# Kernel optimization log

Measured on AMD Instinct MI355X. Metric: run time of the kernel, lower is better.

Reference implementation:

```python
import jax, jax.numpy as jnp
import numpy as np

EMBED_DIM = 512
BATCH = 4
SEQ = 4096

def setup_inputs() -> dict:
    key = jax.random.key(0)
    k1, k2, k3, k4 = jax.random.split(key, 4)
    inputs = jax.random.normal(k1, (BATCH, SEQ, EMBED_DIM), dtype=jnp.float32)
    scale = 1.0 / np.sqrt(EMBED_DIM)
    Wq = jax.random.normal(k2, (EMBED_DIM, EMBED_DIM), dtype=jnp.float32) * scale
    Wk = jax.random.normal(k3, (EMBED_DIM, EMBED_DIM), dtype=jnp.float32) * scale
    Wv = jax.random.normal(k4, (EMBED_DIM, EMBED_DIM), dtype=jnp.float32) * scale
    temperature = jnp.float32(1.0)
    return {"inputs": inputs, "Wq": Wq, "Wk": Wk, "Wv": Wv, "temperature": temperature}

def reference(inputs, Wq, Wk, Wv, temperature):
    # nn.Linear with weight W computes x @ W.T; we store W as (out,in)-equivalent square,
    # applied as x @ W.T for faithfulness.
    Q = jnp.einsum('bsd,ed->bse', inputs, Wq)
    K = jnp.einsum('bsd,ed->bse', inputs, Wk)
    V = jnp.einsum('bsd,ed->bse', inputs, Wv)
    d = inputs.shape[-1]
    scores = jnp.einsum('bqe,bke->bqk', Q, K) * (temperature / jnp.sqrt(jnp.float32(d)))  # [B,S,S]
    attn = jax.nn.softmax(scores, axis=-1)
    return jnp.einsum('bqk,bke->bqe', attn, V)
```

## Files before the change

### kernel.cpp

```cpp
#include <hip/hip_runtime.h>
#include <hip/hip_bf16.h>
#include <stdint.h>

typedef __bf16 bf16;
typedef bf16 bf16x8 __attribute__((ext_vector_type(8)));
typedef bf16 bf16x4 __attribute__((ext_vector_type(4)));
typedef float f32x4 __attribute__((ext_vector_type(4)));

#define MFMA16(a, b, c) __builtin_amdgcn_mfma_f32_16x16x32_bf16((a), (b), (c), 0, 0, 0)

__device__ __forceinline__ void async_ld16(bf16* lds, const bf16* g) {
    __builtin_amdgcn_global_load_lds(
        (const __attribute__((address_space(1))) void*)g,
        (__attribute__((address_space(3))) void*)lds, 16, 0, 0);
}

__global__ __launch_bounds__(256) void proj_kernel(
    const float* __restrict__ X,
    const float* __restrict__ Wq,
    const float* __restrict__ Wk,
    const float* __restrict__ Wv,
    bf16* __restrict__ Qo,
    bf16* __restrict__ Ko,
    bf16* __restrict__ Vt)
{
    __shared__ bf16 As[128][72];
    __shared__ bf16 Bs[128][72];

    const int z    = blockIdx.z;
    const float* W = (z == 0) ? Wq : (z == 1) ? Wk : Wv;
    const int row0 = blockIdx.x * 128;
    const int col0 = blockIdx.y * 128;

    const int t    = threadIdx.x;
    const int w    = t >> 6;
    const int lane = t & 63;
    const int lg   = lane >> 4;
    const int lc   = lane & 15;
    const int wr   = (w >> 1) * 64;
    const int wc   = (w & 1) * 64;

    const int srow = t >> 1;
    const int sd0  = (t & 1) * 16;

    f32x4 acc[4][4];
    for (int a = 0; a < 4; ++a)
        for (int b = 0; b < 4; ++b)
            acc[a][b] = (f32x4){0.f, 0.f, 0.f, 0.f};

    for (int kt = 0; kt < 16; ++kt) {
        const int k = kt * 32;
        __syncthreads();
        {
            const float* xs = X + (size_t)(row0 + srow) * 512 + k + sd0;
            float4 a0 = *(const float4*)(xs + 0);
            float4 a1 = *(const float4*)(xs + 4);
            float4 a2 = *(const float4*)(xs + 8);
            float4 a3 = *(const float4*)(xs + 12);
            bf16x8 h0 = { (bf16)a0.x, (bf16)a0.y, (bf16)a0.z, (bf16)a0.w,
                          (bf16)a1.x, (bf16)a1.y, (bf16)a1.z, (bf16)a1.w };
            bf16x8 h1 = { (bf16)a2.x, (bf16)a2.y, (bf16)a2.z, (bf16)a2.w,
                          (bf16)a3.x, (bf16)a3.y, (bf16)a3.z, (bf16)a3.w };
            *(bf16x8*)&As[srow][sd0]     = h0;
            *(bf16x8*)&As[srow][sd0 + 8] = h1;

            const float* ws_ = W + (size_t)(col0 + srow) * 512 + k + sd0;
            float4 b0 = *(const float4*)(ws_ + 0);
            float4 b1 = *(const float4*)(ws_ + 4);
            float4 b2 = *(const float4*)(ws_ + 8);
            float4 b3 = *(const float4*)(ws_ + 12);
            bf16x8 g0 = { (bf16)b0.x, (bf16)b0.y, (bf16)b0.z, (bf16)b0.w,
                          (bf16)b1.x, (bf16)b1.y, (bf16)b1.z, (bf16)b1.w };
            bf16x8 g1 = { (bf16)b2.x, (bf16)b2.y, (bf16)b2.z, (bf16)b2.w,
                          (bf16)b3.x, (bf16)b3.y, (bf16)b3.z, (bf16)b3.w };
            *(bf16x8*)&Bs[srow][sd0]     = g0;
            *(bf16x8*)&Bs[srow][sd0 + 8] = g1;
        }
        __syncthreads();

        bf16x8 af[4], bfr[4];
        for (int fr = 0; fr < 4; ++fr)
            af[fr] = *(const bf16x8*)&As[wr + fr * 16 + lc][lg * 8];
        for (int fc = 0; fc < 4; ++fc)
            bfr[fc] = *(const bf16x8*)&Bs[wc + fc * 16 + lc][lg * 8];
        for (int fr = 0; fr < 4; ++fr)
            for (int fc = 0; fc < 4; ++fc)
                acc[fr][fc] = MFMA16(af[fr], bfr[fc], acc[fr][fc]);
    }

    if (z < 2) {
        bf16* outp = (z == 0) ? Qo : Ko;
        for (int fr = 0; fr < 4; ++fr)
            for (int fc = 0; fc < 4; ++fc) {
                const int colg = col0 + wc + fc * 16 + lc;
                const int rowb = row0 + wr + fr * 16 + lg * 4;
                for (int i = 0; i < 4; ++i)
                    outp[(size_t)(rowb + i) * 512 + colg] = (bf16)acc[fr][fc][i];
            }
    } else {
        for (int fr = 0; fr < 4; ++fr)
            for (int fc = 0; fc < 4; ++fc) {
                const int e    = col0 + wc + fc * 16 + lc;
                const int rowb = row0 + wr + fr * 16 + lg * 4;
                const int bb   = rowb >> 12;
                const int sl   = rowb & 4095;
                bf16x4 v = { (bf16)acc[fr][fc][0], (bf16)acc[fr][fc][1],
                             (bf16)acc[fr][fc][2], (bf16)acc[fr][fc][3] };
                *(bf16x4*)&Vt[(((size_t)(bb * 512 + e)) << 12) + sl] = v;
            }
    }
}

__global__ __launch_bounds__(512) void flash_kernel(
    const bf16* __restrict__ Q,
    const bf16* __restrict__ K,
    const bf16* __restrict__ Vt,
    const float* __restrict__ temp,
    float* __restrict__ Out)
{
    extern __shared__ char smem[];
    bf16* Kb = (bf16*)smem;
    bf16* Pb = (bf16*)(smem + 2 * 64 * 512 * 2);
    __shared__ float l_part[64][2];

    const int b  = blockIdx.y;
    const int q0 = blockIdx.x * 64;
    const int t    = threadIdx.x;
    const int w    = t >> 6;
    const int lane = t & 63;
    const int lg   = lane >> 4;
    const int lc   = lane & 15;
    const int qrb  = (w >> 1) * 16;
    const int par  = w & 1;

    const float scale2 = temp[0] * 0.04419417382415922f * 1.4426950408889634f;

    const bf16* kbase = K  + (size_t)b * 4096 * 512;
    const bf16* vbase = Vt + (size_t)b * 512 * 4096;

    bf16x8 qf[16];
    {
        const bf16* qrow = Q + ((size_t)(b * 4096 + q0 + qrb + lc)) * 512 + lg * 8;
#pragma unroll
        for (int kt = 0; kt < 16; ++kt)
            qf[kt] = *(const bf16x8*)(qrow + kt * 32);
    }

    f32x4 acc[4][4];
    for (int a = 0; a < 4; ++a)
        for (int c = 0; c < 4; ++c)
            acc[a][c] = (f32x4){0.f, 0.f, 0.f, 0.f};
    float Lacc[4] = {0.f, 0.f, 0.f, 0.f};

#pragma unroll
    for (int j = 0; j < 8; ++j) {
        const int r = w * 8 + j;
        async_ld16(Kb + (size_t)r * 512,
                   kbase + (size_t)r * 512 + ((lane ^ j) << 3));
    }
    __syncthreads();

    const int r7  = lc & 7;
    const int xlo = (lg ^ (r7 & 3)) << 3;
    const int xb2 = (r7 & 4) << 3;

    for (int kv0 = 0; kv0 < 4096; kv0 += 64) {
        const int cur = (kv0 >> 6) & 1;
        const bf16* Kc = Kb + (size_t)cur * 32768;
        bf16*       Pc = Pb + (size_t)cur * (64 * 72);

        if (kv0 + 64 < 4096) {
            bf16* Kn = Kb + (size_t)(cur ^ 1) * 32768;
            const bf16* knx = kbase + (size_t)(kv0 + 64) * 512;
#pragma unroll
            for (int j = 0; j < 8; ++j) {
                const int r = w * 8 + j;
                async_ld16(Kn + (size_t)r * 512,
                           knx + (size_t)r * 512 + ((lane ^ j) << 3));
            }
        }

        const bf16* vb0 = vbase + (size_t)(w * 64 + lc) * 4096 + kv0 + lg * 8;
        bf16x8 vv[8];
#pragma unroll
        for (int kk2 = 0; kk2 < 2; ++kk2)
#pragma unroll
            for (int fc = 0; fc < 4; ++fc)
                vv[kk2 * 4 + fc] =
                    *(const bf16x8*)(vb0 + (size_t)fc * 16 * 4096 + kk2 * 32);

        f32x4 s0 = (f32x4){0.f, 0.f, 0.f, 0.f};
        f32x4 s1 = (f32x4){0.f, 0.f, 0.f, 0.f};
        const bf16* kr0 = Kc + (size_t)(par * 32 + lc) * 512 + xlo;
        const bf16* kr1 = kr0 + (size_t)16 * 512;
#pragma unroll
        for (int kt = 0; kt < 16; ++kt) {
            const int off = (kt * 32) ^ xb2;
            bf16x8 k0 = *(const bf16x8*)(kr0 + off);
            bf16x8 k1 = *(const bf16x8*)(kr1 + off);
            s0 = MFMA16(qf[kt], k0, s0);
            s1 = MFMA16(qf[kt], k1, s1);
        }

#pragma unroll
        for (int i = 0; i < 4; ++i) {
            const int row = qrb + lg * 4 + i;
            float p0 = __builtin_amdgcn_exp2f(s0[i] * scale2);
            float p1 = __builtin_amdgcn_exp2f(s1[i] * scale2);
            Pc[row * 72 + par * 32 + lc]      = (bf16)p0;
            Pc[row * 72 + par * 32 + 16 + lc] = (bf16)p1;
            Lacc[i] += p0 + p1;
        }

        __syncthreads();

#pragma unroll
        for (int kk2 = 0; kk2 < 2; ++kk2) {
            bf16x8 pa[4];
#pragma unroll
            for (int fr = 0; fr < 4; ++fr)
                pa[fr] = *(const bf16x8*)&Pc[(fr * 16 + lc) * 72 + kk2 * 32 + lg * 8];
#pragma unroll
            for (int fc = 0; fc < 4; ++fc)
#pragma unroll
                for (int fr = 0; fr < 4; ++fr)
                    acc[fr][fc] = MFMA16(pa[fr], vv[kk2 * 4 + fc], acc[fr][fc]);
        }
    }

#pragma unroll
    for (int d = 1; d < 16; d <<= 1)
#pragma unroll
        for (int i = 0; i < 4; ++i)
            Lacc[i] += __shfl_xor(Lacc[i], d);
    if (lc == 0)
#pragma unroll
        for (int i = 0; i < 4; ++i)
            l_part[qrb + lg * 4 + i][par] = Lacc[i];
    __syncthreads();

    for (int fr = 0; fr < 4; ++fr) {
        float invl[4];
#pragma unroll
        for (int i = 0; i < 4; ++i) {
            const int row = fr * 16 + lg * 4 + i;
            invl[i] = 1.0f / (l_part[row][0] + l_part[row][1]);
        }
        for (int fc = 0; fc < 4; ++fc) {
            const size_t base =
                ((size_t)(b * 4096 + q0 + fr * 16 + lg * 4)) * 512 + w * 64 + fc * 16 + lc;
#pragma unroll
            for (int i = 0; i < 4; ++i)
                Out[base + (size_t)i * 512] = acc[fr][fc][i] * invl[i];
        }
    }
}

extern "C" void kernel_launch(void* const* d_in, const int* in_sizes, int n_in,
                              void* d_out, int out_size, void* d_ws, size_t ws_size,
                              hipStream_t stream) {
    const float* X    = (const float*)d_in[0];
    const float* Wq   = (const float*)d_in[1];
    const float* Wk   = (const float*)d_in[2];
    const float* Wv   = (const float*)d_in[3];
    const float* temp = (const float*)d_in[4];
    float* Out = (float*)d_out;

    const size_t NE = (size_t)4 * 4096 * 512;
    bf16* Qw = (bf16*)d_ws;
    bf16* Kw = Qw + NE;
    bf16* Vt = Kw + NE;

    proj_kernel<<<dim3(128, 4, 3), 256, 0, stream>>>(X, Wq, Wk, Wv, Qw, Kw, Vt);

    const size_t smem_bytes = (size_t)2 * 64 * 512 * 2 + (size_t)2 * 64 * 72 * 2;
    flash_kernel<<<dim3(64, 4), 512, smem_bytes, stream>>>(Qw, Kw, Vt, temp, Out);
}
```

Baseline: 281.3 us.

## Remap flash blocks across XCDs and replace syncthreads with targeted waitcnt barriers

Flattens the flash grid to 1D and remaps block index to (batch, q-tile) so that blocks sharing a batch's K/V land on the same XCDs, for better L2 reuse. It replaces the full __syncthreads with explicit vmcnt/lgkmcnt waits plus s_barrier, so the V register loads and the next K prefetch stay in flight across the barrier. It also issues the first K tile load before the Q fragment loads and shrinks the P buffer to a single copy. The prefetch is now unconditional, so the last iteration wastes one K tile load, and correctness depends on the hand-counted vmcnt value.

Measured after the change: 308.2 us. 9.6% more time.

```diff
diff --git a/kernel.cpp b/kernel.cpp
--- a/kernel.cpp
+++ b/kernel.cpp
@@ -123,8 +123,10 @@
     bf16* Pb = (bf16*)(smem + 2 * 64 * 512 * 2);
     __shared__ float l_part[64][2];
 
-    const int b  = blockIdx.y;
-    const int q0 = blockIdx.x * 64;
+    const int L  = blockIdx.x;
+    const int b  = (L & 7) >> 1;
+    const int q0 = (((L & 1) << 5) + (L >> 3)) << 6;
+
     const int t    = threadIdx.x;
     const int w    = t >> 6;
     const int lane = t & 63;
@@ -138,6 +140,13 @@
     const bf16* kbase = K  + (size_t)b * 4096 * 512;
     const bf16* vbase = Vt + (size_t)b * 512 * 4096;
 
+#pragma unroll
+    for (int j = 0; j < 8; ++j) {
+        const int r = w * 8 + j;
+        async_ld16(Kb + (size_t)r * 512,
+                   kbase + (size_t)r * 512 + ((lane ^ j) << 3));
+    }
+
     bf16x8 qf[16];
     {
         const bf16* qrow = Q + ((size_t)(b * 4096 + q0 + qrb + lc)) * 512 + lg * 8;
@@ -152,26 +161,29 @@
             acc[a][c] = (f32x4){0.f, 0.f, 0.f, 0.f};
     float Lacc[4] = {0.f, 0.f, 0.f, 0.f};
 
-#pragma unroll
-    for (int j = 0; j < 8; ++j) {
-        const int r = w * 8 + j;
-        async_ld16(Kb + (size_t)r * 512,
-                   kbase + (size_t)r * 512 + ((lane ^ j) << 3));
-    }
     __syncthreads();
 
     const int r7  = lc & 7;
     const int xlo = (lg ^ (r7 & 3)) << 3;
     const int xb2 = (r7 & 4) << 3;
 
-    for (int kv0 = 0; kv0 < 4096; kv0 += 64) {
-        const int cur = (kv0 >> 6) & 1;
+    for (int it = 0; it < 64; ++it) {
+        const int cur = it & 1;
         const bf16* Kc = Kb + (size_t)cur * 32768;
-        bf16*       Pc = Pb + (size_t)cur * (64 * 72);
-
-        if (kv0 + 64 < 4096) {
+
+        const bf16* vb0 = vbase + (size_t)(w * 64 + lc) * 4096 + it * 64 + lg * 8;
+        bf16x8 vv[8];
+#pragma unroll
+        for (int kk2 = 0; kk2 < 2; ++kk2)
+#pragma unroll
+            for (int fc = 0; fc < 4; ++fc)
+                vv[kk2 * 4 + fc] =
+                    *(const bf16x8*)(vb0 + (size_t)fc * 16 * 4096 + kk2 * 32);
+
+        {
+            const int nxt = (it + 1) & 63;
             bf16* Kn = Kb + (size_t)(cur ^ 1) * 32768;
-            const bf16* knx = kbase + (size_t)(kv0 + 64) * 512;
+            const bf16* knx = kbase + (size_t)nxt * 64 * 512;
 #pragma unroll
             for (int j = 0; j < 8; ++j) {
                 const int r = w * 8 + j;
@@ -180,14 +192,8 @@
             }
         }
 
-        const bf16* vb0 = vbase + (size_t)(w * 64 + lc) * 4096 + kv0 + lg * 8;
-        bf16x8 vv[8];
-#pragma unroll
-        for (int kk2 = 0; kk2 < 2; ++kk2)
-#pragma unroll
-            for (int fc = 0; fc < 4; ++fc)
-                vv[kk2 * 4 + fc] =
-                    *(const bf16x8*)(vb0 + (size_t)fc * 16 * 4096 + kk2 * 32);
+        asm volatile("s_waitcnt vmcnt(16)" ::: "memory");
+        __builtin_amdgcn_s_barrier();
 
         f32x4 s0 = (f32x4){0.f, 0.f, 0.f, 0.f};
         f32x4 s1 = (f32x4){0.f, 0.f, 0.f, 0.f};
@@ -207,19 +213,20 @@
             const int row = qrb + lg * 4 + i;
             float p0 = __builtin_amdgcn_exp2f(s0[i] * scale2);
             float p1 = __builtin_amdgcn_exp2f(s1[i] * scale2);
-            Pc[row * 72 + par * 32 + lc]      = (bf16)p0;
-            Pc[row * 72 + par * 32 + 16 + lc] = (bf16)p1;
+            Pb[row * 72 + par * 32 + lc]      = (bf16)p0;
+            Pb[row * 72 + par * 32 + 16 + lc] = (bf16)p1;
             Lacc[i] += p0 + p1;
         }
 
-        __syncthreads();
+        asm volatile("s_waitcnt lgkmcnt(0)" ::: "memory");
+        __builtin_amdgcn_s_barrier();
 
 #pragma unroll
         for (int kk2 = 0; kk2 < 2; ++kk2) {
             bf16x8 pa[4];
 #pragma unroll
             for (int fr = 0; fr < 4; ++fr)
-                pa[fr] = *(const bf16x8*)&Pc[(fr * 16 + lc) * 72 + kk2 * 32 + lg * 8];
+                pa[fr] = *(const bf16x8*)&Pb[(fr * 16 + lc) * 72 + kk2 * 32 + lg * 8];
 #pragma unroll
             for (int fc = 0; fc < 4; ++fc)
 #pragma unroll
@@ -273,6 +280,6 @@
 
     proj_kernel<<<dim3(128, 4, 3), 256, 0, stream>>>(X, Wq, Wk, Wv, Qw, Kw, Vt);
 
-    const size_t smem_bytes = (size_t)2 * 64 * 512 * 2 + (size_t)2 * 64 * 72 * 2;
-    flash_kernel<<<dim3(64, 4), 512, smem_bytes, stream>>>(Qw, Kw, Vt, temp, Out);
-}
+    const size_t smem_bytes = (size_t)2 * 64 * 512 * 2 + (size_t)64 * 72 * 2;
+    flash_kernel<<<dim3(256), 512, smem_bytes, stream>>>(Qw, Kw, Vt, temp, Out);
+}
```

## Warp-specialize flash kernel into QK/softmax producer and PV consumer wavefronts

Applied to the files above, without the earlier changes.

Splits the 8 wavefronts into two groups. Four waves compute QK^T scores, exponentiate and write P tiles to double-buffered LDS while streaming K. The other four consume the previous P tile and multiply it by V, with each holding a wider 4x8 accumulator tile. The aim is to overlap the score/exp phase with the PV MFMA phase across the two groups. In exchange, each group carries more per-wave work and registers (a 128-entry accumulator in the PV waves), and the hand-placed waitcnt and barrier pairing between the groups is fragile.

Measured after the change: 286.6 us. About the same (+1.9%).

```diff
diff --git a/kernel.cpp b/kernel.cpp
--- a/kernel.cpp
+++ b/kernel.cpp
@@ -121,7 +121,7 @@
     extern __shared__ char smem[];
     bf16* Kb = (bf16*)smem;
     bf16* Pb = (bf16*)(smem + 2 * 64 * 512 * 2);
-    __shared__ float l_part[64][2];
+    __shared__ float l_part[64];
 
     const int b  = blockIdx.y;
     const int q0 = blockIdx.x * 64;
@@ -130,128 +130,154 @@
     const int lane = t & 63;
     const int lg   = lane >> 4;
     const int lc   = lane & 15;
-    const int qrb  = (w >> 1) * 16;
-    const int par  = w & 1;
 
     const float scale2 = temp[0] * 0.04419417382415922f * 1.4426950408889634f;
 
     const bf16* kbase = K  + (size_t)b * 4096 * 512;
     const bf16* vbase = Vt + (size_t)b * 512 * 4096;
 
-    bf16x8 qf[16];
-    {
-        const bf16* qrow = Q + ((size_t)(b * 4096 + q0 + qrb + lc)) * 512 + lg * 8;
-#pragma unroll
-        for (int kt = 0; kt < 16; ++kt)
-            qf[kt] = *(const bf16x8*)(qrow + kt * 32);
-    }
-
-    f32x4 acc[4][4];
-    for (int a = 0; a < 4; ++a)
-        for (int c = 0; c < 4; ++c)
-            acc[a][c] = (f32x4){0.f, 0.f, 0.f, 0.f};
-    float Lacc[4] = {0.f, 0.f, 0.f, 0.f};
-
-#pragma unroll
-    for (int j = 0; j < 8; ++j) {
-        const int r = w * 8 + j;
-        async_ld16(Kb + (size_t)r * 512,
-                   kbase + (size_t)r * 512 + ((lane ^ j) << 3));
-    }
-    __syncthreads();
-
-    const int r7  = lc & 7;
-    const int xlo = (lg ^ (r7 & 3)) << 3;
-    const int xb2 = (r7 & 4) << 3;
-
-    for (int kv0 = 0; kv0 < 4096; kv0 += 64) {
-        const int cur = (kv0 >> 6) & 1;
-        const bf16* Kc = Kb + (size_t)cur * 32768;
-        bf16*       Pc = Pb + (size_t)cur * (64 * 72);
-
-        if (kv0 + 64 < 4096) {
-            bf16* Kn = Kb + (size_t)(cur ^ 1) * 32768;
-            const bf16* knx = kbase + (size_t)(kv0 + 64) * 512;
-#pragma unroll
-            for (int j = 0; j < 8; ++j) {
-                const int r = w * 8 + j;
-                async_ld16(Kn + (size_t)r * 512,
-                           knx + (size_t)r * 512 + ((lane ^ j) << 3));
-            }
-        }
-
-        const bf16* vb0 = vbase + (size_t)(w * 64 + lc) * 4096 + kv0 + lg * 8;
-        bf16x8 vv[8];
-#pragma unroll
-        for (int kk2 = 0; kk2 < 2; ++kk2)
+    if (w < 4) {
+#pragma unroll
+        for (int j = 0; j < 16; ++j) {
+            const int r = w * 16 + j;
+            async_ld16(Kb + (size_t)r * 512,
+                       kbase + (size_t)r * 512 + ((lane ^ (j & 7)) << 3));
+        }
+        bf16x8 qf[16];
+        {
+            const bf16* qrow =
+                Q + ((size_t)(b * 4096 + q0 + w * 16 + lc)) * 512 + lg * 8;
+#pragma unroll
+            for (int kt = 0; kt < 16; ++kt)
+                qf[kt] = *(const bf16x8*)(qrow + kt * 32);
+        }
+        float Lacc[4] = {0.f, 0.f, 0.f, 0.f};
+
+        asm volatile("s_waitcnt vmcnt(16)" ::: "memory");
+        __builtin_amdgcn_s_barrier();
+
+        const int r7  = lc & 7;
+        const int xlo = (lg ^ (r7 & 3)) << 3;
+        const int xb2 = (r7 & 4) << 3;
+
+        for (int it = 0; it < 64; ++it) {
+            const int cur = it & 1;
+            const bf16* Kc = Kb + (size_t)cur * 32768;
+            bf16*       Pc = Pb + (size_t)cur * (64 * 72);
+
+            if (it < 63) {
+                bf16* Kn = Kb + (size_t)(cur ^ 1) * 32768;
+                const bf16* knx = kbase + (size_t)(it + 1) * 64 * 512;
+#pragma unroll
+                for (int j = 0; j < 16; ++j) {
+                    const int r = w * 16 + j;
+                    async_ld16(Kn + (size_t)r * 512,
+                               knx + (size_t)r * 512 + ((lane ^ (j & 7)) << 3));
+                }
+            }
+
+            f32x4 s[4];
 #pragma unroll
             for (int fc = 0; fc < 4; ++fc)
-                vv[kk2 * 4 + fc] =
-                    *(const bf16x8*)(vb0 + (size_t)fc * 16 * 4096 + kk2 * 32);
-
-        f32x4 s0 = (f32x4){0.f, 0.f, 0.f, 0.f};
-        f32x4 s1 = (f32x4){0.f, 0.f, 0.f, 0.f};
-        const bf16* kr0 = Kc + (size_t)(par * 32 + lc) * 512 + xlo;
-        const bf16* kr1 = kr0 + (size_t)16 * 512;
-#pragma unroll
-        for (int kt = 0; kt < 16; ++kt) {
-            const int off = (kt * 32) ^ xb2;
-            bf16x8 k0 = *(const bf16x8*)(kr0 + off);
-            bf16x8 k1 = *(const bf16x8*)(kr1 + off);
-            s0 = MFMA16(qf[kt], k0, s0);
-            s1 = MFMA16(qf[kt], k1, s1);
-        }
-
-#pragma unroll
-        for (int i = 0; i < 4; ++i) {
-            const int row = qrb + lg * 4 + i;
-            float p0 = __builtin_amdgcn_exp2f(s0[i] * scale2);
-            float p1 = __builtin_amdgcn_exp2f(s1[i] * scale2);
-            Pc[row * 72 + par * 32 + lc]      = (bf16)p0;
-            Pc[row * 72 + par * 32 + 16 + lc] = (bf16)p1;
-            Lacc[i] += p0 + p1;
-        }
-
+                s[fc] = (f32x4){0.f, 0.f, 0.f, 0.f};
+            const bf16* kr0 = Kc + (size_t)lc * 512 + xlo;
+#pragma unroll
+            for (int kt = 0; kt < 16; ++kt) {
+                const int off = (kt * 32) ^ xb2;
+#pragma unroll
+                for (int fc = 0; fc < 4; ++fc) {
+                    bf16x8 kf = *(const bf16x8*)(kr0 + (size_t)fc * 8192 + off);
+                    s[fc] = MFMA16(qf[kt], kf, s[fc]);
+                }
+            }
+
+#pragma unroll
+            for (int fc = 0; fc < 4; ++fc)
+#pragma unroll
+                for (int i = 0; i < 4; ++i) {
+                    float p = __builtin_amdgcn_exp2f(s[fc][i] * scale2);
+                    Pc[(w * 16 + lg * 4 + i) * 72 + fc * 16 + lc] = (bf16)p;
+                    Lacc[i] += p;
+                }
+
+            asm volatile("s_waitcnt lgkmcnt(0) vmcnt(0)" ::: "memory");
+            __builtin_amdgcn_s_barrier();
+        }
+
+#pragma unroll
+        for (int d = 1; d < 16; d <<= 1)
+#pragma unroll
+            for (int i = 0; i < 4; ++i)
+                Lacc[i] += __shfl_xor(Lacc[i], d);
+        if (lc == 0)
+#pragma unroll
+            for (int i = 0; i < 4; ++i)
+                l_part[w * 16 + lg * 4 + i] = Lacc[i];
         __syncthreads();
-
-#pragma unroll
-        for (int kk2 = 0; kk2 < 2; ++kk2) {
-            bf16x8 pa[4];
-#pragma unroll
-            for (int fr = 0; fr < 4; ++fr)
-                pa[fr] = *(const bf16x8*)&Pc[(fr * 16 + lc) * 72 + kk2 * 32 + lg * 8];
-#pragma unroll
-            for (int fc = 0; fc < 4; ++fc)
-#pragma unroll
-                for (int fr = 0; fr < 4; ++fr)
-                    acc[fr][fc] = MFMA16(pa[fr], vv[kk2 * 4 + fc], acc[fr][fc]);
-        }
-    }
-
-#pragma unroll
-    for (int d = 1; d < 16; d <<= 1)
-#pragma unroll
-        for (int i = 0; i < 4; ++i)
-            Lacc[i] += __shfl_xor(Lacc[i], d);
-    if (lc == 0)
-#pragma unroll
-        for (int i = 0; i < 4; ++i)
-            l_part[qrb + lg * 4 + i][par] = Lacc[i];
-    __syncthreads();
-
-    for (int fr = 0; fr < 4; ++fr) {
-        float invl[4];
-#pragma unroll
-        for (int i = 0; i < 4; ++i) {
-            const int row = fr * 16 + lg * 4 + i;
-            invl[i] = 1.0f / (l_part[row][0] + l_part[row][1]);
-        }
-        for (int fc = 0; fc < 4; ++fc) {
-            const size_t base =
-                ((size_t)(b * 4096 + q0 + fr * 16 + lg * 4)) * 512 + w * 64 + fc * 16 + lc;
+    } else {
+        const int wB = w - 4;
+        f32x4 acc[4][8];
+#pragma unroll
+        for (int a = 0; a < 4; ++a)
+#pragma unroll
+            for (int c = 0; c < 8; ++c)
+                acc[a][c] = (f32x4){0.f, 0.f, 0.f, 0.f};
+
+        __builtin_amdgcn_s_barrier();
+
+#define PV_TILE(J)                                                             \
+        {                                                                      \
+            const bf16* Pc  = Pb + (size_t)((J) & 1) * (64 * 72);              \
+            const bf16* vb0 = vbase + (size_t)(wB * 128 + lc) * 4096           \
+                              + (J) * 64 + lg * 8;                             \
+            bf16x8 vvA[8], vvB[8];                                             \
+            _Pragma("unroll")                                                  \
+            for (int fc = 0; fc < 8; ++fc) {                                   \
+                vvA[fc] = *(const bf16x8*)(vb0 + (size_t)fc * 16 * 4096);      \
+                vvB[fc] = *(const bf16x8*)(vb0 + (size_t)fc * 16 * 4096 + 32); \
+            }                                                                  \
+            bf16x8 pa[4];                                                      \
+            _Pragma("unroll")                                                  \
+            for (int fr = 0; fr < 4; ++fr)                                     \
+                pa[fr] = *(const bf16x8*)&Pc[(fr * 16 + lc) * 72 + lg * 8];    \
+            _Pragma("unroll")                                                  \
+            for (int fc = 0; fc < 8; ++fc)                                     \
+                _Pragma("unroll")                                              \
+                for (int fr = 0; fr < 4; ++fr)                                 \
+                    acc[fr][fc] = MFMA16(pa[fr], vvA[fc], acc[fr][fc]);        \
+            _Pragma("unroll")                                                  \
+            for (int fr = 0; fr < 4; ++fr)                                     \
+                pa[fr] = *(const bf16x8*)&Pc[(fr * 16 + lc) * 72 + 32 + lg * 8]; \
+            _Pragma("unroll")                                                  \
+            for (int fc = 0; fc < 8; ++fc)                                     \
+                _Pragma("unroll")                                              \
+                for (int fr = 0; fr < 4; ++fr)                                 \
+                    acc[fr][fc] = MFMA16(pa[fr], vvB[fc], acc[fr][fc]);        \
+        }
+
+        for (int it = 0; it < 64; ++it) {
+            if (it > 0) PV_TILE(it - 1)
+            asm volatile("s_waitcnt lgkmcnt(0)" ::: "memory");
+            __builtin_amdgcn_s_barrier();
+        }
+        PV_TILE(63)
+#undef PV_TILE
+
+        __syncthreads();
+
+        for (int fr = 0; fr < 4; ++fr) {
+            float invl[4];
 #pragma unroll
             for (int i = 0; i < 4; ++i)
-                Out[base + (size_t)i * 512] = acc[fr][fc][i] * invl[i];
+                invl[i] = 1.0f / l_part[fr * 16 + lg * 4 + i];
+            for (int fc = 0; fc < 8; ++fc) {
+                const size_t base =
+                    ((size_t)(b * 4096 + q0 + fr * 16 + lg * 4)) * 512 +
+                    wB * 128 + fc * 16 + lc;
+#pragma unroll
+                for (int i = 0; i < 4; ++i)
+                    Out[base + (size_t)i * 512] = acc[fr][fc][i] * invl[i];
+            }
         }
     }
 }
```
